# Kernel tuning notes

Measured on AMD Instinct MI355X. Metric: run time of the kernel, lower is better.

The kernel has to match this reference:

```python
import jax, jax.numpy as jnp
import numpy as np
from jax import lax

DIM = 256
NUM_HEADS = 8
HEAD_DIM = DIM // NUM_HEADS
SCALE = HEAD_DIM ** -0.5


def _avg_pool(x, k, p):
    # torch AvgPool2d(kernel=k, stride=1, padding=p) with count_include_pad=True
    s = lax.reduce_window(x, 0.0, lax.add,
                          window_dimensions=(1, 1, k, k),
                          window_strides=(1, 1, 1, 1),
                          padding=((0, 0), (0, 0), (p, p), (p, p)))
    return s / (k * k)


def setup_inputs() -> dict:
    key = jax.random.key(0)
    ks = jax.random.split(key, 7)
    x = jax.random.normal(ks[0], (2, DIM, 48, 48), dtype=jnp.float32)
    q_w = jax.random.normal(ks[1], (DIM, DIM), dtype=jnp.float32) * (DIM ** -0.5)
    q_b = jax.random.normal(ks[2], (DIM,), dtype=jnp.float32) * 0.02
    kv_w = jax.random.normal(ks[3], (2 * DIM, DIM), dtype=jnp.float32) * (DIM ** -0.5)
    kv_b = jax.random.normal(ks[4], (2 * DIM,), dtype=jnp.float32) * 0.02
    proj_w = jax.random.normal(ks[5], (DIM, DIM), dtype=jnp.float32) * (DIM ** -0.5)
    proj_b = jax.random.normal(ks[6], (DIM,), dtype=jnp.float32) * 0.02
    return {"x": x, "q_w": q_w, "q_b": q_b, "kv_w": kv_w, "kv_b": kv_b,
            "proj_w": proj_w, "proj_b": proj_b}


def reference(x, q_w, q_b, kv_w, kv_b, proj_w, proj_b):
    B, C, H, W = x.shape
    h, d, N = NUM_HEADS, HEAD_DIM, H * W

    # q = 1x1 conv -> [B, h, N, d]
    q = jnp.einsum('oc,bchw->bohw', q_w, x) + q_b[None, :, None, None]
    q = q.reshape(B, h, d, N).transpose(0, 1, 3, 2)

    # kv is a linear 1x1 conv, so (kv(x)+kv(p1)+kv(p2)+kv(p3))/4 == kv(mean of inputs)
    x_avg = (x + _avg_pool(x, 3, 1) + _avg_pool(x, 5, 2) + _avg_pool(x, 7, 3)) / 4.0
    kv = jnp.einsum('oc,bchw->bohw', kv_w, x_avg) + kv_b[None, :, None, None]
    kv = kv.reshape(B, 2, h, d, N).transpose(1, 0, 2, 4, 3)  # [2, B, h, N, d]
    k, v = kv[0], kv[1]

    attn = jnp.einsum('bhnd,bhmd->bhnm', q, k) * SCALE  # [B, h, N, N]
    attn = jax.nn.softmax(attn, axis=-1)
    y = jnp.einsum('bhnm,bhmd->bhnd', attn, v)  # [B, h, N, d]
    # faithful to torch: transpose(1,2) then flat reshape to [B, C, H, W]
    y = y.transpose(0, 2, 1, 3).reshape(B, C, H, W)

    out = jnp.einsum('oc,bchw->bohw', proj_w, y) + proj_b[None, :, None, None]
    return out
```

## Files before the change

kernel.cpp:

```cpp
#include <hip/hip_runtime.h>
#include <hip/hip_bf16.h>
#include <cstdint>

#define DIMC  256
#define NH    8
#define HD    32
#define NPIX  2304
#define BATCH 2
#define NSPLIT 6
#define KPS   384
#define KT    32
#define NT    (KPS / KT)

typedef short s16x8 __attribute__((ext_vector_type(8)));
typedef short s16x4 __attribute__((ext_vector_type(4)));
typedef float f32x4 __attribute__((ext_vector_type(4)));

#define MFMA32(A,B,C) __builtin_amdgcn_mfma_f32_16x16x32_bf16(A,B,C,0,0,0)

__device__ inline uint32_t rnau(float x) { return __float_as_uint(x) + 0x8000u; }
__device__ inline uint32_t pk2(uint32_t l_, uint32_t h_) {
  return __builtin_amdgcn_perm(h_, l_, 0x07060302u);
}

__global__ __launch_bounds__(256) void pool_kernel(const float* __restrict__ x,
                                                   float* __restrict__ xavg) {
  const int plane = blockIdx.x;
  const float* xp = x + (size_t)plane * NPIX;
  __shared__ float sx[NPIX];
  __shared__ float h3[NPIX], h5[NPIX], h7[NPIX];
  const int t = threadIdx.x;
#pragma unroll
  for (int r = 0; r < 9; ++r) sx[r * 256 + t] = xp[r * 256 + t];
  __syncthreads();
#pragma unroll
  for (int r = 0; r < 9; ++r) {
    int p = r * 256 + t;
    int i = p / 48, j = p - i * 48;
    float a3 = 0.f, a5 = 0.f, a7 = 0.f;
#pragma unroll
    for (int dj = -3; dj <= 3; ++dj) {
      int jj = j + dj;
      if (jj < 0 || jj >= 48) continue;
      float v = sx[i * 48 + jj];
      a7 += v;
      if (dj >= -2 && dj <= 2) a5 += v;
      if (dj >= -1 && dj <= 1) a3 += v;
    }
    h3[p] = a3; h5[p] = a5; h7[p] = a7;
  }
  __syncthreads();
#pragma unroll
  for (int r = 0; r < 9; ++r) {
    int p = r * 256 + t;
    int i = p / 48, j = p - i * 48;
    float b3 = 0.f, b5 = 0.f, b7 = 0.f;
#pragma unroll
    for (int di = -3; di <= 3; ++di) {
      int ii = i + di;
      if (ii < 0 || ii >= 48) continue;
      int q = ii * 48 + j;
      b7 += h7[q];
      if (di >= -2 && di <= 2) b5 += h5[q];
      if (di >= -1 && di <= 1) b3 += h3[q];
    }
    xavg[(size_t)plane * NPIX + p] =
        0.25f * (sx[p] + b3 * (1.f / 9.f) + b5 * (1.f / 25.f) + b7 * (1.f / 49.f));
  }
}

__global__ __launch_bounds__(256) void conv_all(
    const float* __restrict__ x, const float* __restrict__ xavg,
    const float* __restrict__ qw, const float* __restrict__ kvw,
    const float* __restrict__ pw_,
    short* __restrict__ Xh, short* __restrict__ Ah,
    short* __restrict__ Wth) {
  const int bx = blockIdx.x;
  const int t = threadIdx.x;
  if (bx < 576) {
    const float* src = (bx < 288) ? x : xavg;
    short* dhi = (bx < 288) ? Xh : Ah;
    const int bb = (bx < 288) ? bx : bx - 288;
    const int n0 = (bb % 36) * 64, c0 = ((bb / 36) & 3) * 64, b = bb / 144;
    __shared__ __align__(16) float T[64][68];
    {
      const int c = t >> 2, n4 = (t & 3) * 16;
      const float* sp = src + ((size_t)b * DIMC + c0 + c) * NPIX + n0 + n4;
#pragma unroll
      for (int i2 = 0; i2 < 4; ++i2)
        *(f32x4*)&T[c][n4 + i2 * 4] = *(const f32x4*)(sp + i2 * 4);
    }
    __syncthreads();
    {
      const int n = t >> 2, c4 = (t & 3) * 16;
      float v[16];
#pragma unroll
      for (int i = 0; i < 16; ++i) v[i] = T[c4 + i][n];
      uint32_t a[16];
#pragma unroll
      for (int i = 0; i < 16; ++i) a[i] = rnau(v[i]);
      union { s16x8 s; uint32_t u[4]; } H0, H1;
#pragma unroll
      for (int j = 0; j < 4; ++j) {
        H0.u[j] = pk2(a[2 * j], a[2 * j + 1]);
        H1.u[j] = pk2(a[8 + 2 * j], a[8 + 2 * j + 1]);
      }
      const size_t off = ((size_t)b * NPIX + n0 + n) * DIMC + c0 + c4;
      *(s16x8*)(dhi + off) = H0.s; *(s16x8*)(dhi + off + 8) = H1.s;
    }
  } else {
    const int idx = ((bx - 576) * 256 + t) * 8;
    const float* s;
    int off;
    if (idx < 65536)       { s = qw;  off = idx; }
    else if (idx < 196608) { s = kvw; off = idx - 65536; }
    else                   { s = pw_; off = idx - 196608; }
    f32x4 x0 = *(const f32x4*)(s + off);
    f32x4 x1 = *(const f32x4*)(s + off + 4);
    float v[8] = {x0[0], x0[1], x0[2], x0[3], x1[0], x1[1], x1[2], x1[3]};
    uint32_t a[8];
#pragma unroll
    for (int i = 0; i < 8; ++i) a[i] = rnau(v[i]);
    union { s16x8 s; uint32_t u[4]; } H;
#pragma unroll
    for (int j = 0; j < 4; ++j) H.u[j] = pk2(a[2 * j], a[2 * j + 1]);
    *(s16x8*)(Wth + idx) = H.s;
  }
}

__global__ __launch_bounds__(128) void gemm_proj_hi(
    const short* __restrict__ Wh,
    const float* __restrict__ bias,
    const short* __restrict__ Zh,
    float* __restrict__ out) {
  __shared__ __align__(16) float Cl[32][68];
  const int n0 = blockIdx.x * 64;
  const int o0 = blockIdx.y * 32;
  const int b  = blockIdx.z;
  const int tid = threadIdx.x;
  const int wave = tid >> 6, lane = tid & 63;
  const int g = lane >> 4, q = lane & 15;

  const short* wph = Wh + ((o0 + wave * 16 + q) * DIMC + g * 8);
  const short* iph = Zh + ((size_t)(b * NPIX + n0 + q) * DIMC + g * 8);

  f32x4 acc[4] = {{0,0,0,0},{0,0,0,0},{0,0,0,0},{0,0,0,0}};
#pragma unroll
  for (int c0 = 0; c0 < DIMC; c0 += 32) {
    s16x8 ah = *(const s16x8*)(wph + c0);
#pragma unroll
    for (int st = 0; st < 4; ++st) {
      s16x8 bh_ = *(const s16x8*)(iph + (size_t)st * 16 * DIMC + c0);
      acc[st] = MFMA32(ah, bh_, acc[st]);
    }
  }
#pragma unroll
  for (int st = 0; st < 4; ++st)
#pragma unroll
    for (int r = 0; r < 4; ++r)
      Cl[wave * 16 + g * 4 + r][st * 16 + q] = acc[st][r];
  __syncthreads();

  const int o = tid >> 2, nc = (tid & 3) * 16;
  const float bv = bias[o0 + o];
  float* op = out + ((size_t)b * DIMC + o0 + o) * NPIX + n0 + nc;
#pragma unroll
  for (int i2 = 0; i2 < 4; ++i2) {
    f32x4 v = *(const f32x4*)&Cl[o][nc + i2 * 4];
    v[0] += bv; v[1] += bv; v[2] += bv; v[3] += bv;
    *(f32x4*)(op + i2 * 4) = v;
  }
}

__global__ __launch_bounds__(128) void gemm_qkv_hi(
    const short* __restrict__ Wth,
    const float* __restrict__ q_b, const float* __restrict__ kv_b,
    const short* __restrict__ Xh, const short* __restrict__ Ah,
    short* __restrict__ Qhi, short* __restrict__ Khi, short* __restrict__ Vhi,
    float qscale) {
  __shared__ __align__(16) float Cl[32][68];
  const int by = blockIdx.y;
  const bool isQ = (by < 8);
  const int o0 = isQ ? by * 32 : (by - 8) * 32;
  const short* Wh = isQ ? Wth : Wth + 65536;
  const float* bias = isQ ? q_b : kv_b;
  const short* Inh = isQ ? Xh : Ah;
  const float scale = isQ ? qscale : 1.0f;
  short* d1 = isQ ? Qhi : Khi;
  const int n0 = blockIdx.x * 64;
  const int b  = blockIdx.z;

  const int tid = threadIdx.x;
  const int wave = tid >> 6, lane = tid & 63;
  const int g = lane >> 4, q = lane & 15;

  const short* wph = Wh + ((o0 + wave * 16 + q) * DIMC + g * 8);
  const short* iph = Inh + ((size_t)(b * NPIX + n0 + q) * DIMC + g * 8);

  f32x4 acc[4] = {{0,0,0,0},{0,0,0,0},{0,0,0,0},{0,0,0,0}};
#pragma unroll
  for (int c0 = 0; c0 < DIMC; c0 += 32) {
    s16x8 ah = *(const s16x8*)(wph + c0);
#pragma unroll
    for (int st = 0; st < 4; ++st) {
      s16x8 bh_ = *(const s16x8*)(iph + (size_t)st * 16 * DIMC + c0);
      acc[st] = MFMA32(ah, bh_, acc[st]);
    }
  }
#pragma unroll
  for (int st = 0; st < 4; ++st)
#pragma unroll
    for (int r = 0; r < 4; ++r)
      Cl[wave * 16 + g * 4 + r][st * 16 + q] = acc[st][r];
  __syncthreads();

  if (o0 < 256) {
    const int n = tid >> 1, oq = tid & 1;
    const int h = o0 >> 5;
    const float* bp = bias + o0 + oq * 16;
    float v[16];
#pragma unroll
    for (int i = 0; i < 16; ++i) v[i] = (Cl[oq * 16 + i][n] + bp[i]) * scale;
    uint32_t a[16];
#pragma unroll
    for (int i = 0; i < 16; ++i) a[i] = rnau(v[i]);
    union { s16x8 s; uint32_t u[4]; } H0, H1;
#pragma unroll
    for (int j = 0; j < 4; ++j) {
      H0.u[j] = pk2(a[2 * j], a[2 * j + 1]);
      H1.u[j] = pk2(a[8 + 2 * j], a[8 + 2 * j + 1]);
    }
    const size_t off = ((size_t)((b * 8 + h) * NPIX + n0 + n)) * HD + oq * 16;
    *(s16x8*)(d1 + off) = H0.s; *(s16x8*)(d1 + off + 8) = H1.s;
  } else {
    const int o = tid >> 2, nc = (tid & 3) * 16;
    const int h = (o0 - 256) >> 5;
    const float bv = bias[o0 + o];
    float v[16];
#pragma unroll
    for (int i2 = 0; i2 < 4; ++i2) {
      f32x4 t4 = *(const f32x4*)&Cl[o][nc + i2 * 4];
      v[i2 * 4 + 0] = t4[0] + bv; v[i2 * 4 + 1] = t4[1] + bv;
      v[i2 * 4 + 2] = t4[2] + bv; v[i2 * 4 + 3] = t4[3] + bv;
    }
    uint32_t a[16];
#pragma unroll
    for (int i = 0; i < 16; ++i) a[i] = rnau(v[i]);
    union { s16x8 s; uint32_t u[4]; } H0, H1;
#pragma unroll
    for (int j = 0; j < 4; ++j) {
      H0.u[j] = pk2(a[2 * j], a[2 * j + 1]);
      H1.u[j] = pk2(a[8 + 2 * j], a[8 + 2 * j + 1]);
    }
    const size_t off = ((size_t)((b * 8 + h) * HD + o)) * NPIX + n0 + nc;
    *(s16x8*)(Vhi + off) = H0.s; *(s16x8*)(Vhi + off + 8) = H1.s;
  }
}

__global__ __launch_bounds__(128) void attn_mfma(
    const short* __restrict__ Qhi,
    const short* __restrict__ Khi,
    const short* __restrict__ Vhi,
    short* __restrict__ part_o,
    float* __restrict__ part_l) {
  const int sb = blockIdx.x;
  const int bh = sb / 36;
  const int qb = sb % 36;
  const int split = blockIdx.y;
  const int tid = threadIdx.x;
  const int wave = tid >> 6, lane = tid & 63;
  const int g = lane >> 4, q = lane & 15;
  const int base = qb * 64 + wave * 32;

  __shared__ __align__(16) short Plds[2][2][16 * 40];
  short* pwA = &Plds[wave][0][0];
  short* pwB = &Plds[wave][1][0];

  const size_t qoff = ((size_t)bh * NPIX + base + q) * HD + g * 8;
  const s16x8 qhA = *(const s16x8*)(Qhi + qoff);
  const s16x8 qhB = *(const s16x8*)(Qhi + qoff + 16 * HD);

  const short* kp = Khi + ((size_t)bh * NPIX + split * KPS + q) * HD + g * 8;
  const short* vp = Vhi + ((size_t)bh * HD + q) * NPIX + split * KPS + g * 8;

  const f32x4 Z4 = {0.f, 0.f, 0.f, 0.f};
  f32x4 OA0 = Z4, OA1 = Z4, OB0 = Z4, OB1 = Z4;
  f32x4 LA = Z4, LB = Z4;
  s16x8 kb[3][2], vb[3][2], pfA, pfB, vp0, vp1;

  union { s16x8 s; uint32_t u[4]; } ONE;
  ONE.u[0] = 0x3F803F80u; ONE.u[1] = 0x3F803F80u;
  ONE.u[2] = 0x3F803F80u; ONE.u[3] = 0x3F803F80u;
  const s16x8 ones = ONE.s;

  kb[0][0] = *(const s16x8*)(kp);
  kb[0][1] = *(const s16x8*)(kp + 16 * HD);
  vb[0][0] = *(const s16x8*)(vp);
  vb[0][1] = *(const s16x8*)(vp + 16 * NPIX);
  kb[1][0] = *(const s16x8*)(kp + KT * HD);
  kb[1][1] = *(const s16x8*)(kp + KT * HD + 16 * HD);
  vb[1][0] = *(const s16x8*)(vp + KT);
  vb[1][1] = *(const s16x8*)(vp + KT + 16 * NPIX);

#pragma unroll
  for (int t = 0; t < NT; ++t) {
    const int cur = t % 3;
    if (t + 2 < NT) {
      const int nx2 = (t + 2) % 3;
      const short* kpn = kp + (t + 2) * (KT * HD);
      const short* vpn = vp + (t + 2) * KT;
      kb[nx2][0] = *(const s16x8*)(kpn);
      kb[nx2][1] = *(const s16x8*)(kpn + 16 * HD);
      vb[nx2][0] = *(const s16x8*)(vpn);
      vb[nx2][1] = *(const s16x8*)(vpn + 16 * NPIX);
    }
    f32x4 SA0 = MFMA32(kb[cur][0], qhA, Z4);
    f32x4 SA1 = MFMA32(kb[cur][1], qhA, Z4);
    f32x4 SB0 = MFMA32(kb[cur][0], qhB, Z4);
    f32x4 SB1 = MFMA32(kb[cur][1], qhB, Z4);
    if (t > 0) {
      OA0 = MFMA32(vp0, pfA, OA0);
      OA1 = MFMA32(vp1, pfA, OA1);
      OB0 = MFMA32(vp0, pfB, OB0);
      OB1 = MFMA32(vp1, pfB, OB1);
      LA  = MFMA32(ones, pfA, LA);
      LB  = MFMA32(ones, pfB, LB);
    }
    {
      f32x4 p0, p1;
#pragma unroll
      for (int r = 0; r < 4; ++r) { p0[r] = exp2f(SA0[r]); p1[r] = exp2f(SA1[r]); }
      uint2 w0, w1;
      w0.x = pk2(rnau(p0[0]), rnau(p0[1])); w0.y = pk2(rnau(p0[2]), rnau(p0[3]));
      w1.x = pk2(rnau(p1[0]), rnau(p1[1])); w1.y = pk2(rnau(p1[2]), rnau(p1[3]));
      *(uint2*)&pwA[q * 40 + g * 4] = w0;
      *(uint2*)&pwA[q * 40 + 16 + g * 4] = w1;
    }
    {
      f32x4 p0, p1;
#pragma unroll
      for (int r = 0; r < 4; ++r) { p0[r] = exp2f(SB0[r]); p1[r] = exp2f(SB1[r]); }
      uint2 w0, w1;
      w0.x = pk2(rnau(p0[0]), rnau(p0[1])); w0.y = pk2(rnau(p0[2]), rnau(p0[3]));
      w1.x = pk2(rnau(p1[0]), rnau(p1[1])); w1.y = pk2(rnau(p1[2]), rnau(p1[3]));
      *(uint2*)&pwB[q * 40 + g * 4] = w0;
      *(uint2*)&pwB[q * 40 + 16 + g * 4] = w1;
    }
    vp0 = vb[cur][0]; vp1 = vb[cur][1];
    pfA = *(const s16x8*)&pwA[q * 40 + g * 8];
    pfB = *(const s16x8*)&pwB[q * 40 + g * 8];
  }
  OA0 = MFMA32(vp0, pfA, OA0);
  OA1 = MFMA32(vp1, pfA, OA1);
  OB0 = MFMA32(vp0, pfB, OB0);
  OB1 = MFMA32(vp1, pfB, OB1);
  LA  = MFMA32(ones, pfA, LA);
  LB  = MFMA32(ones, pfB, LB);

  const int rowA = bh * NPIX + base + q;
  const int rowB = rowA + 16;
  short* poA = part_o + ((size_t)rowA * NSPLIT + split) * HD;
  short* poB = part_o + ((size_t)rowB * NSPLIT + split) * HD;
  uint2 wa0, wa1, wb0, wb1;
  wa0.x = pk2(rnau(OA0[0]), rnau(OA0[1])); wa0.y = pk2(rnau(OA0[2]), rnau(OA0[3]));
  wa1.x = pk2(rnau(OA1[0]), rnau(OA1[1])); wa1.y = pk2(rnau(OA1[2]), rnau(OA1[3]));
  wb0.x = pk2(rnau(OB0[0]), rnau(OB0[1])); wb0.y = pk2(rnau(OB0[2]), rnau(OB0[3]));
  wb1.x = pk2(rnau(OB1[0]), rnau(OB1[1])); wb1.y = pk2(rnau(OB1[2]), rnau(OB1[3]));
  *(uint2*)(poA + g * 4)      = wa0;
  *(uint2*)(poA + 16 + g * 4) = wa1;
  *(uint2*)(poB + g * 4)      = wb0;
  *(uint2*)(poB + 16 + g * 4) = wb1;
  if (g == 0) {
    part_l[(size_t)rowA * NSPLIT + split] = LA[0];
    part_l[(size_t)rowB * NSPLIT + split] = LB[0];
  }
}

__global__ __launch_bounds__(288) void attn_merge(const short* __restrict__ part_o,
                                                  const float* __restrict__ part_l,
                                                  short* __restrict__ zh) {
  const int blk = blockIdx.x;
  const int bh = blk >> 4;
  const int n0 = (blk & 15) * 144;
  const int head = bh & 7, b = bh >> 3;
  const int t = threadIdx.x;
  __shared__ __align__(16) float T[144][36];
  {
    const int r = t >> 1, uh = (t & 1) * 4;
    const int idx = bh * NPIX + n0 + r;
    const float* pl = part_l + (size_t)idx * NSPLIT;
    float L = 0.f;
#pragma unroll
    for (int s = 0; s < NSPLIT; ++s) L += pl[s];
    const float inv = 1.f / L;
    const short* po = part_o + (size_t)idx * (NSPLIT * HD);
#pragma unroll
    for (int u = 0; u < 4; ++u) {
      f32x4 v = {0.f, 0.f, 0.f, 0.f};
#pragma unroll
      for (int s = 0; s < NSPLIT; ++s) {
        const uint2 w = *(const uint2*)(po + s * HD + (uh + u) * 4);
        v[0] += __uint_as_float(w.x << 16);
        v[1] += __uint_as_float(w.x & 0xffff0000u);
        v[2] += __uint_as_float(w.y << 16);
        v[3] += __uint_as_float(w.y & 0xffff0000u);
      }
      v[0] *= inv; v[1] *= inv; v[2] *= inv; v[3] *= inv;
      *(f32x4*)&T[r][(uh + u) * 4] = v;
    }
  }
  __syncthreads();
  {
    const int r9 = t / 32, dd = t & 31;
    const int p = r9 * 256 + head * HD + dd;
    const int c0 = n0 / 9;
    float v[16];
#pragma unroll
    for (int j = 0; j < 16; ++j) v[j] = T[9 * j + r9][dd];
    uint32_t a[16];
#pragma unroll
    for (int j = 0; j < 16; ++j) a[j] = rnau(v[j]);
    const size_t off = ((size_t)b * NPIX + p) * DIMC + c0;
#pragma unroll
    for (int c8 = 0; c8 < 2; ++c8) {
      union { s16x8 s; uint32_t u[4]; } H;
#pragma unroll
      for (int j = 0; j < 4; ++j)
        H.u[j] = pk2(a[c8 * 8 + 2 * j], a[c8 * 8 + 2 * j + 1]);
      *(s16x8*)(zh + off + c8 * 8) = H.s;
    }
  }
}

extern "C" void kernel_launch(void* const* d_in, const int* in_sizes, int n_in,
                              void* d_out, int out_size, void* d_ws, size_t ws_size,
                              hipStream_t stream) {
  const float* x      = (const float*)d_in[0];
  const float* q_w    = (const float*)d_in[1];
  const float* q_b    = (const float*)d_in[2];
  const float* kv_w   = (const float*)d_in[3];
  const float* kv_b   = (const float*)d_in[4];
  const float* proj_w = (const float*)d_in[5];
  const float* proj_b = (const float*)d_in[6];
  float* out = (float*)d_out;

  char* w = (char*)d_ws;
  float* xavg = (float*)w;
  short* Xh   = (short*)(w + 4718592);
  short* Ah   = (short*)(w + 9437184);
  short* part_o = (short*)w;
  short* Wth  = (short*)(w + 28311552);
  short* Qhi  = (short*)(w + 29360128);
  short* Khi  = (short*)(w + 31719424);
  short* Vhi  = (short*)(w + 34078720);
  float* part_l = (float*)(w + 36438016);
  short* Zh   = (short*)(w + 37322752);

  const float qscale = 0.17677669529663689f * 1.4426950408889634f;

  pool_kernel<<<BATCH * DIMC, 256, 0, stream>>>(x, xavg);
  conv_all<<<704, 256, 0, stream>>>(x, xavg, q_w, kv_w, proj_w, Xh, Ah, Wth);
  gemm_qkv_hi<<<dim3(36, 24, 2), 128, 0, stream>>>(Wth, q_b, kv_b,
                                                   Xh, Ah, Qhi, Khi, Vhi, qscale);
  attn_mfma<<<dim3(16 * 36, NSPLIT), 128, 0, stream>>>(Qhi, Khi, Vhi, part_o, part_l);
  attn_merge<<<256, 288, 0, stream>>>(part_o, part_l, Zh);
  gemm_proj_hi<<<dim3(36, 8, 2), 128, 0, stream>>>(Wth + 196608, proj_b, Zh, out);
}
```

Before: 149.2 us.

## Fuse split-attention merge into output projection GEMM

```diff
diff --git a/kernel.cpp b/kernel.cpp
--- a/kernel.cpp
+++ b/kernel.cpp
@@ -128,50 +128,6 @@
   }
 }
 
-__global__ __launch_bounds__(128) void gemm_proj_hi(
-    const short* __restrict__ Wh,
-    const float* __restrict__ bias,
-    const short* __restrict__ Zh,
-    float* __restrict__ out) {
-  __shared__ __align__(16) float Cl[32][68];
-  const int n0 = blockIdx.x * 64;
-  const int o0 = blockIdx.y * 32;
-  const int b  = blockIdx.z;
-  const int tid = threadIdx.x;
-  const int wave = tid >> 6, lane = tid & 63;
-  const int g = lane >> 4, q = lane & 15;
-
-  const short* wph = Wh + ((o0 + wave * 16 + q) * DIMC + g * 8);
-  const short* iph = Zh + ((size_t)(b * NPIX + n0 + q) * DIMC + g * 8);
-
-  f32x4 acc[4] = {{0,0,0,0},{0,0,0,0},{0,0,0,0},{0,0,0,0}};
-#pragma unroll
-  for (int c0 = 0; c0 < DIMC; c0 += 32) {
-    s16x8 ah = *(const s16x8*)(wph + c0);
-#pragma unroll
-    for (int st = 0; st < 4; ++st) {
-      s16x8 bh_ = *(const s16x8*)(iph + (size_t)st * 16 * DIMC + c0);
-      acc[st] = MFMA32(ah, bh_, acc[st]);
-    }
-  }
-#pragma unroll
-  for (int st = 0; st < 4; ++st)
-#pragma unroll
-    for (int r = 0; r < 4; ++r)
-      Cl[wave * 16 + g * 4 + r][st * 16 + q] = acc[st][r];
-  __syncthreads();
-
-  const int o = tid >> 2, nc = (tid & 3) * 16;
-  const float bv = bias[o0 + o];
-  float* op = out + ((size_t)b * DIMC + o0 + o) * NPIX + n0 + nc;
-#pragma unroll
-  for (int i2 = 0; i2 < 4; ++i2) {
-    f32x4 v = *(const f32x4*)&Cl[o][nc + i2 * 4];
-    v[0] += bv; v[1] += bv; v[2] += bv; v[3] += bv;
-    *(f32x4*)(op + i2 * 4) = v;
-  }
-}
-
 __global__ __launch_bounds__(128) void gemm_qkv_hi(
     const short* __restrict__ Wth,
     const float* __restrict__ q_b, const float* __restrict__ kv_b,
@@ -376,59 +332,86 @@
   }
 }
 
-__global__ __launch_bounds__(288) void attn_merge(const short* __restrict__ part_o,
-                                                  const float* __restrict__ part_l,
-                                                  short* __restrict__ zh) {
-  const int blk = blockIdx.x;
-  const int bh = blk >> 4;
-  const int n0 = (blk & 15) * 144;
-  const int head = bh & 7, b = bh >> 3;
-  const int t = threadIdx.x;
-  __shared__ __align__(16) float T[144][36];
+__global__ __launch_bounds__(256) void proj_fused(
+    const short* __restrict__ Wh,
+    const float* __restrict__ bias,
+    const short* __restrict__ part_o,
+    const float* __restrict__ part_l,
+    float* __restrict__ out) {
+  const int n0 = blockIdx.x * 64;
+  const int o0 = blockIdx.y * 64;
+  const int b  = blockIdx.z;
+  const int r9 = n0 >> 8;
+  const int h0 = (n0 & 255) >> 5;
+  const int tid = threadIdx.x;
+
+  __shared__ __align__(16) short Zt[64][272];
+  __shared__ float Li[256][2];
+  __shared__ __align__(16) float Cl[64][68];
+
+  for (int e = tid; e < 512; e += 256) {
+    const int c = e >> 1, hh = e & 1;
+    const float* pl = part_l +
+        ((size_t)(b * 8 + h0 + hh) * NPIX + 9 * c + r9) * NSPLIT;
+    Li[c][hh] = 1.f / (pl[0] + pl[1] + pl[2] + pl[3] + pl[4] + pl[5]);
+  }
+  __syncthreads();
+
   {
-    const int r = t >> 1, uh = (t & 1) * 4;
-    const int idx = bh * NPIX + n0 + r;
-    const float* pl = part_l + (size_t)idx * NSPLIT;
-    float L = 0.f;
-#pragma unroll
-    for (int s = 0; s < NSPLIT; ++s) L += pl[s];
-    const float inv = 1.f / L;
-    const short* po = part_o + (size_t)idx * (NSPLIT * HD);
-#pragma unroll
-    for (int u = 0; u < 4; ++u) {
-      f32x4 v = {0.f, 0.f, 0.f, 0.f};
-#pragma unroll
-      for (int s = 0; s < NSPLIT; ++s) {
-        const uint2 w = *(const uint2*)(po + s * HD + (uh + u) * 4);
-        v[0] += __uint_as_float(w.x << 16);
-        v[1] += __uint_as_float(w.x & 0xffff0000u);
-        v[2] += __uint_as_float(w.y << 16);
-        v[3] += __uint_as_float(w.y & 0xffff0000u);
+    const int dd = tid & 63, qq = tid >> 6;
+    const int hh = dd >> 5, d = dd & 31;
+    const short* pob = part_o +
+        ((size_t)(b * 8 + h0 + hh) * NPIX) * (NSPLIT * HD) + d;
+#pragma unroll
+    for (int cg = 0; cg < 8; ++cg) {
+      const int cb = qq * 64 + cg * 8;
+      uint32_t a[8];
+#pragma unroll
+      for (int j = 0; j < 8; ++j) {
+        const int c = cb + j;
+        const short* po = pob + (size_t)(9 * c + r9) * (NSPLIT * HD);
+        float acc = 0.f;
+#pragma unroll
+        for (int s = 0; s < NSPLIT; ++s)
+          acc += __uint_as_float(((uint32_t)(unsigned short)po[s * HD]) << 16);
+        a[j] = rnau(acc * Li[c][hh]);
       }
-      v[0] *= inv; v[1] *= inv; v[2] *= inv; v[3] *= inv;
-      *(f32x4*)&T[r][(uh + u) * 4] = v;
-    }
-  }
-  __syncthreads();
-  {
-    const int r9 = t / 32, dd = t & 31;
-    const int p = r9 * 256 + head * HD + dd;
-    const int c0 = n0 / 9;
-    float v[16];
-#pragma unroll
-    for (int j = 0; j < 16; ++j) v[j] = T[9 * j + r9][dd];
-    uint32_t a[16];
-#pragma unroll
-    for (int j = 0; j < 16; ++j) a[j] = rnau(v[j]);
-    const size_t off = ((size_t)b * NPIX + p) * DIMC + c0;
-#pragma unroll
-    for (int c8 = 0; c8 < 2; ++c8) {
       union { s16x8 s; uint32_t u[4]; } H;
 #pragma unroll
-      for (int j = 0; j < 4; ++j)
-        H.u[j] = pk2(a[c8 * 8 + 2 * j], a[c8 * 8 + 2 * j + 1]);
-      *(s16x8*)(zh + off + c8 * 8) = H.s;
-    }
+      for (int j2 = 0; j2 < 4; ++j2) H.u[j2] = pk2(a[2 * j2], a[2 * j2 + 1]);
+      *(s16x8*)&Zt[dd][cb] = H.s;
+    }
+  }
+  __syncthreads();
+
+  const int wave = tid >> 6, lane = tid & 63;
+  const int g = lane >> 4, q = lane & 15;
+  const short* wph = Wh + ((o0 + wave * 16 + q) * DIMC + g * 8);
+  f32x4 acc[4] = {{0,0,0,0},{0,0,0,0},{0,0,0,0},{0,0,0,0}};
+#pragma unroll
+  for (int c0 = 0; c0 < DIMC; c0 += 32) {
+    s16x8 ah = *(const s16x8*)(wph + c0);
+#pragma unroll
+    for (int st = 0; st < 4; ++st) {
+      s16x8 bh_ = *(const s16x8*)&Zt[st * 16 + q][c0 + g * 8];
+      acc[st] = MFMA32(ah, bh_, acc[st]);
+    }
+  }
+#pragma unroll
+  for (int st = 0; st < 4; ++st)
+#pragma unroll
+    for (int r = 0; r < 4; ++r)
+      Cl[wave * 16 + g * 4 + r][st * 16 + q] = acc[st][r];
+  __syncthreads();
+
+  const int o = tid >> 2, nc = (tid & 3) * 16;
+  const float bv = bias[o0 + o];
+  float* op = out + ((size_t)b * DIMC + o0 + o) * NPIX + n0 + nc;
+#pragma unroll
+  for (int i2 = 0; i2 < 4; ++i2) {
+    f32x4 v = *(const f32x4*)&Cl[o][nc + i2 * 4];
+    v[0] += bv; v[1] += bv; v[2] += bv; v[3] += bv;
+    *(f32x4*)(op + i2 * 4) = v;
   }
 }
 
@@ -454,7 +437,6 @@
   short* Khi  = (short*)(w + 31719424);
   short* Vhi  = (short*)(w + 34078720);
   float* part_l = (float*)(w + 36438016);
-  short* Zh   = (short*)(w + 37322752);
 
   const float qscale = 0.17677669529663689f * 1.4426950408889634f;
 
@@ -463,6 +445,6 @@
   gemm_qkv_hi<<<dim3(36, 24, 2), 128, 0, stream>>>(Wth, q_b, kv_b,
                                                    Xh, Ah, Qhi, Khi, Vhi, qscale);
   attn_mfma<<<dim3(16 * 36, NSPLIT), 128, 0, stream>>>(Qhi, Khi, Vhi, part_o, part_l);
-  attn_merge<<<256, 288, 0, stream>>>(part_o, part_l, Zh);
-  gemm_proj_hi<<<dim3(36, 8, 2), 128, 0, stream>>>(Wth + 196608, proj_b, Zh, out);
-}
+  proj_fused<<<dim3(36, 4, 2), 256, 0, stream>>>(Wth + 196608, proj_b,
+                                                 part_o, part_l, out);
+}
```

Measured after the change: 150.1 us. Within noise of the previous version (+0.5%).
